# Kernel tuning notes

Hardware: AMD Instinct MI355X
Metric: run time of the kernel (lower is better)

## Reference

```python
import jax, jax.numpy as jnp
import numpy as np

B, S, D, H, DFF = 2, 2048, 768, 12, 3072
DK = D // H
EPS = 1e-6
NEG = -1e9


def setup_inputs() -> dict:
    key = jax.random.key(0)
    ks = jax.random.split(key, 16)
    s = 1.0 / np.sqrt(D)
    inp = {
        'x': jax.random.normal(ks[0], (B, S, D), jnp.float32),
        'wq': jax.random.normal(ks[1], (D, D), jnp.float32) * s,
        'bq': jnp.zeros((D,), jnp.float32),
        'wk': jax.random.normal(ks[2], (D, D), jnp.float32) * s,
        'bk': jnp.zeros((D,), jnp.float32),
        'wv': jax.random.normal(ks[3], (D, D), jnp.float32) * s,
        'bv': jnp.zeros((D,), jnp.float32),
        'wo': jax.random.normal(ks[4], (D, D), jnp.float32) * s,
        'bo': jnp.zeros((D,), jnp.float32),
        'w1': jax.random.normal(ks[5], (D, DFF), jnp.float32) * s,
        'b1': jnp.zeros((DFF,), jnp.float32),
        'w2': jax.random.normal(ks[6], (DFF, D), jnp.float32) * (1.0 / np.sqrt(DFF)),
        'b2': jnp.zeros((D,), jnp.float32),
        'alpha1': jnp.ones((1,), jnp.float32),
        'beta1': jnp.zeros((1,), jnp.float32),
        'alpha2': jnp.ones((1,), jnp.float32),
        'beta2': jnp.zeros((1,), jnp.float32),
        'mask': jax.random.randint(ks[7], (1, 1, S, S), 0, 2, jnp.int32),
    }
    return inp


def layernorm(x, alpha, beta):
    # torch: mean and UNBIASED std (ddof=1), eps added to std (not variance)
    mean = jnp.mean(x, axis=-1, keepdims=True)
    std = jnp.std(x, axis=-1, keepdims=True, ddof=1)
    return alpha * (x - mean) / (std + EPS) + beta


def encoder_layer(x, wq, bq, wk, bk, wv, bv, wo, bo, w1, b1, w2, b2,
                  alpha1, beta1, alpha2, beta2, mask):
    # projections -> [B, H, S, DK]
    def split_heads(t):
        return t.reshape(B, S, H, DK).transpose(0, 2, 1, 3)
    q = split_heads(x @ wq + bq)
    k = split_heads(x @ wk + bk)
    v = split_heads(x @ wv + bv)
    scores = jnp.einsum('bhqd,bhkd->bhqk', q, k) / np.sqrt(DK)  # [B,H,S,S]
    scores = jnp.where(mask == 0, NEG, scores)
    attn = jax.nn.softmax(scores, axis=-1)
    ctx = jnp.einsum('bhqk,bhkd->bhqd', attn, v)
    ctx = ctx.transpose(0, 2, 1, 3).reshape(B, S, D)
    attn_out = ctx @ wo + bo
    x = layernorm(x + attn_out, alpha1, beta1)
    ff = jax.nn.relu(x @ w1 + b1) @ w2 + b2
    x = layernorm(x + ff, alpha2, beta2)
    return x


def reference(x, wq, bq, wk, bk, wv, bv, wo, bo, w1, b1, w2, b2,
              alpha1, beta1, alpha2, beta2, mask):
    return encoder_layer(x, wq, bq, wk, bk, wv, bv, wo, bo, w1, b1, w2, b2,
                         alpha1, beta1, alpha2, beta2, mask)
```

## Files before the change

### kernel.cpp

```cpp
#include <hip/hip_runtime.h>
#include <hip/hip_bf16.h>


typedef short short8 __attribute__((ext_vector_type(8)));
typedef float floatx4 __attribute__((ext_vector_type(4)));
typedef unsigned short ushort_t;
typedef ushort_t ushort4_t __attribute__((ext_vector_type(4)));

#define B_ 2
#define S_ 2048
#define D_ 768
#define H_ 12
#define DK_ 64
#define DFF_ 3072
#define M_ (B_ * S_)
#define RS_ (3 * D_)

#define LOG2E 1.44269504f
#define FMAX_SHIFT 16.0f

__device__ __forceinline__ float bf2f(ushort_t h) {
  union { unsigned int u; float f; } v; v.u = ((unsigned int)h) << 16; return v.f;
}
__device__ __forceinline__ ushort_t f2bf(float f) {
  union { float f; unsigned int u; } v; v.f = f;
  unsigned int u = v.u;
  unsigned int r = (u + 0x7fffu + ((u >> 16) & 1u)) >> 16;
  return (ushort_t)r;
}

__global__ __launch_bounds__(256) void transpose_all_f2b(
    const float* __restrict__ wq, const float* __restrict__ wk,
    const float* __restrict__ wv, const float* __restrict__ wo,
    const float* __restrict__ w1, const float* __restrict__ w2,
    ushort_t* __restrict__ wTqkv, ushort_t* __restrict__ woT,
    ushort_t* __restrict__ w1T, ushort_t* __restrict__ w2T) {
  __shared__ ushort_t t[32][33];
  const int blk = blockIdx.x;
  const float* in; ushort_t* out; int K, N, bx, by;
  if (blk < 2304) {
    const int z = blk / 576, rr = blk % 576;
    in = (z == 0) ? wq : (z == 1) ? wk : (z == 2) ? wv : wo;
    out = (z < 3) ? (wTqkv + (size_t)z * D_ * D_) : woT;
    K = D_; N = D_; bx = rr % 24; by = rr / 24;
  } else if (blk < 4608) {
    const int rr = blk - 2304;
    in = w1; out = w1T; K = D_; N = DFF_; bx = rr % 96; by = rr / 96;
  } else {
    const int rr = blk - 4608;
    in = w2; out = w2T; K = DFF_; N = D_; bx = rr % 24; by = rr / 24;
  }
  const int nt = bx * 32, kt = by * 32;
  const int tx = threadIdx.x & 31, ty = threadIdx.x >> 5;
#pragma unroll
  for (int i = 0; i < 4; i++)
    t[ty + i * 8][tx] = f2bf(in[(size_t)(kt + ty + i * 8) * N + nt + tx]);
  __syncthreads();
#pragma unroll
  for (int i = 0; i < 4; i++)
    out[(size_t)(nt + ty + i * 8) * K + kt + tx] = t[tx][ty + i * 8];
}

__global__ __launch_bounds__(256) void prep_misc(
    const int* __restrict__ mask, ushort_t* __restrict__ maskp,
    const float* __restrict__ x, ushort_t* __restrict__ xb,
    const float* __restrict__ bq, const float* __restrict__ bk,
    const float* __restrict__ bv, float* __restrict__ bqkv) {
  const int blk = blockIdx.x, tid = threadIdx.x;
  if (blk < 2048) {
    const int t = blk * 256 + tid;
    const int q = t >> 8;
    const int cc = t & 255;
    const int k0 = (cc >> 3) * 64;
    const int g = cc & 7, f = g >> 2, lq = g & 3;
    const int* mrow = mask + (size_t)q * S_ + k0;
    const ushort_t cm = f2bf(-1.4427e9f);
    const ushort_t cu = f2bf(-FMAX_SHIFT * LOG2E);
    short8 o;
#pragma unroll
    for (int n2 = 0; n2 < 2; n2++)
#pragma unroll
      for (int r = 0; r < 4; r++) {
        const int kpl = 32 * f + 16 * n2 + 4 * lq + r;
        o[n2 * 4 + r] = (short)((mrow[kpl] == 0) ? cm : cu);
      }
    *(short8*)(maskp + (size_t)q * S_ + k0 + g * 8) = o;
  } else if (blk < 5120) {
    const int i = ((blk - 2048) * 256 + tid) * 4;
#pragma unroll
    for (int j = 0; j < 4; j++) xb[i + j] = f2bf(x[i + j]);
  } else {
    const int i = (blk - 5120) * 256 + tid;
    if (i < 3 * D_)
      bqkv[i] = (i < D_) ? bq[i] : (i < 2 * D_ ? bk[i - D_] : bv[i - 2 * D_]);
  }
}

__global__ __launch_bounds__(256) void vtrans(
    const ushort_t* __restrict__ qkv, ushort_t* __restrict__ vt) {
  __shared__ __align__(16) ushort_t T[64 * 72];
  const int tid = threadIdx.x;
  const int bh = blockIdx.y, b = bh / H_, h = bh % H_;
  const int k0 = blockIdx.x * 64;
  const ushort_t* vbase = qkv + (size_t)(b * S_) * RS_ + 2 * D_ + h * DK_;
#pragma unroll
  for (int i = 0; i < 2; i++) {
    const int idx = tid + i * 256;
    const int r = idx >> 3, c = idx & 7;
    short8 vv = *(const short8*)(vbase + (size_t)(k0 + r) * RS_ + c * 8);
    const int sw = (r >> 3) ^ c;
#pragma unroll
    for (int j = 0; j < 8; j++)
      T[(c * 8 + j) * 72 + sw * 8 + (r & 7)] = (ushort_t)vv[j];
  }
  __syncthreads();
#pragma unroll
  for (int i = 0; i < 2; i++) {
    const int ch = tid + i * 256;
    const int d = ch >> 3, g = ch & 7, f = g >> 2, lq = g & 3;
    short8 o;
#pragma unroll
    for (int n2 = 0; n2 < 2; n2++)
#pragma unroll
      for (int r = 0; r < 4; r++) {
        const int kpl = 32 * f + 16 * n2 + 4 * lq + r;
        o[n2 * 4 + r] = (short)T[d * 72 + (((kpl >> 3) ^ (d >> 3)) * 8) + (kpl & 7)];
      }
    *(short8*)(vt + ((size_t)bh * 64 + d) * S_ + k0 + g * 8) = o;
  }
}

template <int BN, bool SPLIT>
__global__ __launch_bounds__(256) void gemm_bt_t(
    const ushort_t* __restrict__ A, const ushort_t* __restrict__ Bt,
    const float* __restrict__ bias, void* __restrict__ Cv,
    int M, int N, int K, int relu, int qcols, float qscale) {
  constexpr int WN = (BN == 128) ? 2 : 1;
  constexpr int WM = 4 / WN;
  constexpr int FI = 128 / WM / 16;
  constexpr int FJ = BN / WN / 16;
  constexpr int Z = SPLIT ? 2 : 1;
  __shared__ __align__(16) ushort_t Al[2][128 * 32];
  __shared__ __align__(16) ushort_t Bl[2][BN * 32];
  const int tid = threadIdx.x;
  const int w = tid >> 6, lane = tid & 63;
  const int wm = (WN == 2) ? (w >> 1) : w;
  const int wn = (WN == 2) ? (w & 1) : 0;
  const int lq = lane >> 4, lr = lane & 15;

  const int NT_n = N / BN;
  const int mg = M >> 10;
  const int lin = blockIdx.x;
  const int xcd = lin & 7, idx = lin >> 3;
  const int m_t = xcd * mg + idx / (NT_n * Z);
  const int rem = idx % (NT_n * Z);
  const int n_t = rem % NT_n;
  const int z   = rem / NT_n;
  const int m0 = m_t * 128, n0 = n_t * BN;

  int kBeg = 0, kEnd = K;
  if (SPLIT) { const int half = K >> 1; kBeg = z * half; kEnd = kBeg + half; }
  const int NT = (kEnd - kBeg) / 32;

  auto stage = [&](int kt, int s) {
    const int k0 = kBeg + kt * 32;
#pragma unroll
    for (int i = 0; i < 2; i++) {
      const int base = (w * 2 + i) * 512;
      const int e = base + lane * 8;
      const int row = e >> 5, col = e & 31;
      __builtin_amdgcn_global_load_lds(
          (const __attribute__((address_space(1))) void*)(A + (size_t)(m0 + row) * K + k0 + col),
          (__attribute__((address_space(3))) void*)(&Al[s][base]), 16, 0, 0);
    }
#pragma unroll
    for (int i = 0; i < BN / 64; i++) {
      const int base = (w * (BN / 64) + i) * 512;
      const int e = base + lane * 8;
      const int row = e >> 5, col = e & 31;
      __builtin_amdgcn_global_load_lds(
          (const __attribute__((address_space(1))) void*)(Bt + (size_t)(n0 + row) * K + k0 + col),
          (__attribute__((address_space(3))) void*)(&Bl[s][base]), 16, 0, 0);
    }
  };

  floatx4 acc[FI][FJ];
#pragma unroll
  for (int i = 0; i < FI; i++)
#pragma unroll
    for (int j = 0; j < FJ; j++) acc[i][j] = (floatx4){0.f, 0.f, 0.f, 0.f};

  stage(0, 0);
  for (int kt = 0; kt < NT; kt++) {
    const int s = kt & 1;
    __syncthreads();
    if (kt + 1 < NT) stage(kt + 1, s ^ 1);

    short8 af[FI], bf[FJ];
#pragma unroll
    for (int i = 0; i < FI; i++)
      af[i] = *(const short8*)&Al[s][(wm * (FI * 16) + i * 16 + lr) * 32 + lq * 8];
#pragma unroll
    for (int j = 0; j < FJ; j++)
      bf[j] = *(const short8*)&Bl[s][(wn * (FJ * 16) + j * 16 + lr) * 32 + lq * 8];
#pragma unroll
    for (int i = 0; i < FI; i++)
#pragma unroll
      for (int j = 0; j < FJ; j++)
        acc[i][j] = __builtin_amdgcn_mfma_f32_16x16x32_bf16(af[i], bf[j], acc[i][j], 0, 0, 0);
  }

#pragma unroll
  for (int i = 0; i < FI; i++) {
    const int m = m0 + wm * (FI * 16) + i * 16 + lq * 4;
#pragma unroll
    for (int j = 0; j < FJ; j++) {
      const int n = n0 + wn * (FJ * 16) + j * 16 + lr;
      if (SPLIT) {
        ushort_t* P = (ushort_t*)Cv + (size_t)z * M * N;
#pragma unroll
        for (int r = 0; r < 4; r++)
          P[(size_t)(m + r) * N + n] = f2bf(acc[i][j][r]);
      } else {
        const float bv = bias[n];
#pragma unroll
        for (int r = 0; r < 4; r++) {
          float v = acc[i][j][r] + bv;
          if (n < qcols) v *= qscale;
          if (relu) v = v > 0.f ? v : 0.f;
          ((ushort_t*)Cv)[(size_t)(m + r) * N + n] = f2bf(v);
        }
      }
    }
  }
}

__global__ __launch_bounds__(256, 3) void flash_attn(
    const ushort_t* __restrict__ qkv, const ushort_t* __restrict__ vt,
    const ushort_t* __restrict__ maskp, ushort_t* __restrict__ ctx) {
  __shared__ __align__(16) ushort_t lds[2][3][64 * 64];
  const int tid = threadIdx.x;
  const int w = tid >> 6, lane = tid & 63;
  const int wq = w >> 1, wk = w & 1;
  const int lq = lane >> 4, lr = lane & 15;
  const int blk = blockIdx.x;
  const int bh = blk % (B_ * H_), qb = blk / (B_ * H_);
  const int b = bh / H_, h = bh % H_;
  const int q0 = qb * 64;
  const ushort_t* qbase = qkv + (size_t)(b * S_) * RS_ + h * DK_;
  const ushort_t* kbase = qbase + D_;
  const ushort_t* vtb   = vt + (size_t)bh * DK_ * S_;
  const ushort_t* mb    = maskp + (size_t)q0 * S_;

  short8 qfr[2][2];
#pragma unroll
  for (int qf = 0; qf < 2; qf++)
#pragma unroll
    for (int f = 0; f < 2; f++)
      qfr[qf][f] = *(const short8*)(
          qbase + (size_t)(q0 + wq * 32 + qf * 16 + lr) * RS_ + f * 32 + lq * 8);

  auto stage = [&](int k0, int s) {
#pragma unroll
    for (int i = 0; i < 2; i++) {
      const int id = i * 256 + tid;
      const int row = id >> 3;
      const int cc = ((id & 7) ^ (row & 7)) * 8;
      const int dbase = (i * 256 + w * 64) * 8;
      __builtin_amdgcn_global_load_lds(
          (const __attribute__((address_space(1))) void*)(kbase + (size_t)(k0 + row) * RS_ + cc),
          (__attribute__((address_space(3))) void*)(&lds[s][0][dbase]), 16, 0, 0);
      __builtin_amdgcn_global_load_lds(
          (const __attribute__((address_space(1))) void*)(vtb + (size_t)row * S_ + k0 + cc),
          (__attribute__((address_space(3))) void*)(&lds[s][1][dbase]), 16, 0, 0);
      __builtin_amdgcn_global_load_lds(
          (const __attribute__((address_space(1))) void*)(mb + (size_t)row * S_ + k0 + cc),
          (__attribute__((address_space(3))) void*)(&lds[s][2][dbase]), 16, 0, 0);
    }
  };

  floatx4 oacc[2][4], oli[2];
#pragma unroll
  for (int qf = 0; qf < 2; qf++) {
    oli[qf] = (floatx4){0.f, 0.f, 0.f, 0.f};
#pragma unroll
    for (int dt = 0; dt < 4; dt++) oacc[qf][dt] = (floatx4){0.f, 0.f, 0.f, 0.f};
  }
  short8 ones;
#pragma unroll
  for (int j = 0; j < 8; j++) ones[j] = (short)0x3F80;

  stage(0, 0);
  __syncthreads();

  const int sw8 = lr & 7;
  const int c0 = (lq ^ sw8) * 8;
  const int c1 = ((4 + lq) ^ sw8) * 8;
  const int cW = ((4 * wk + lq) ^ sw8) * 8;

  constexpr int NT = S_ / 64;
  for (int t = 0; t < NT; t++) {
    const int s = t & 1;
    if (t + 1 < NT) stage((t + 1) * 64, s ^ 1);

    const ushort_t* kl = &lds[s][0][0];
    const ushort_t* vl = &lds[s][1][0];
    const ushort_t* ml = &lds[s][2][0];

    floatx4 sacc[2][2];
#pragma unroll
    for (int qf = 0; qf < 2; qf++) {
      const short8 bb = *(const short8*)(ml + (wq * 32 + qf * 16 + lr) * 64 + cW);
#pragma unroll
      for (int n2 = 0; n2 < 2; n2++)
#pragma unroll
        for (int r = 0; r < 4; r++)
          sacc[qf][n2][r] = bf2f((ushort_t)bb[n2 * 4 + r]);
    }

#pragma unroll
    for (int n2 = 0; n2 < 2; n2++) {
      const int krow = ((2 * wk + n2) * 16 + lr) * 64;
      short8 a0 = *(const short8*)(kl + krow + c0);
      short8 a1 = *(const short8*)(kl + krow + c1);
#pragma unroll
      for (int qf = 0; qf < 2; qf++) {
        sacc[qf][n2] = __builtin_amdgcn_mfma_f32_16x16x32_bf16(a0, qfr[qf][0], sacc[qf][n2], 0, 0, 0);
        sacc[qf][n2] = __builtin_amdgcn_mfma_f32_16x16x32_bf16(a1, qfr[qf][1], sacc[qf][n2], 0, 0, 0);
      }
    }

    short8 pf[2];
#pragma unroll
    for (int qf = 0; qf < 2; qf++) {
      union { __hip_bfloat162 h2[4]; short8 v; } u;
#pragma unroll
      for (int jj = 0; jj < 4; jj++) {
        const int e0 = jj * 2, e1 = jj * 2 + 1;
        float2 p2;
        p2.x = __builtin_amdgcn_exp2f(sacc[qf][e0 >> 2][e0 & 3]);
        p2.y = __builtin_amdgcn_exp2f(sacc[qf][e1 >> 2][e1 & 3]);
        u.h2[jj] = __float22bfloat162_rn(p2);
      }
      pf[qf] = u.v;
    }

#pragma unroll
    for (int dt = 0; dt < 4; dt++) {
      const short8 vfr = *(const short8*)(vl + (dt * 16 + lr) * 64 + cW);
#pragma unroll
      for (int qf = 0; qf < 2; qf++)
        oacc[qf][dt] = __builtin_amdgcn_mfma_f32_16x16x32_bf16(vfr, pf[qf], oacc[qf][dt], 0, 0, 0);
    }
#pragma unroll
    for (int qf = 0; qf < 2; qf++)
      oli[qf] = __builtin_amdgcn_mfma_f32_16x16x32_bf16(ones, pf[qf], oli[qf], 0, 0, 0);

    __syncthreads();
  }

  float* ex = (float*)&lds[0][0][0];
  if (wk == 1) {
    float* dst = ex + (size_t)(wq * 64 + lane) * 37;
#pragma unroll
    for (int qf = 0; qf < 2; qf++)
#pragma unroll
      for (int dt = 0; dt < 4; dt++)
#pragma unroll
        for (int r = 0; r < 4; r++)
          dst[qf * 16 + dt * 4 + r] = oacc[qf][dt][r];
    dst[32] = oli[0][0];
    dst[33] = oli[1][0];
  }
  __syncthreads();
  if (wk == 0) {
    const float* src = ex + (size_t)(wq * 64 + lane) * 37;
#pragma unroll
    for (int qf = 0; qf < 2; qf++)
#pragma unroll
      for (int dt = 0; dt < 4; dt++)
#pragma unroll
        for (int r = 0; r < 4; r++)
          oacc[qf][dt][r] += src[qf * 16 + dt * 4 + r];
    const float inv0 = 1.f / (oli[0][0] + src[32] + 1e-30f);
    const float inv1 = 1.f / (oli[1][0] + src[33] + 1e-30f);
#pragma unroll
    for (int qf = 0; qf < 2; qf++) {
      const float inv = qf ? inv1 : inv0;
      const size_t row = (size_t)(b * S_ + q0 + wq * 32 + qf * 16 + lr) * D_ + h * DK_;
#pragma unroll
      for (int dt = 0; dt < 4; dt++) {
        ushort4_t o;
#pragma unroll
        for (int r = 0; r < 4; r++) o[r] = f2bf(oacc[qf][dt][r] * inv);
        *(ushort4_t*)(ctx + row + dt * 16 + lq * 4) = o;
      }
    }
  }
}

template <bool XF, bool OF>
__global__ __launch_bounds__(256) void add_ln_comb(
    const void* __restrict__ xv, const ushort_t* __restrict__ P0,
    const ushort_t* __restrict__ P1, const float* __restrict__ cb,
    const float* __restrict__ alpha, const float* __restrict__ beta,
    void* __restrict__ outv) {
  const int row = blockIdx.x, tid = threadIdx.x;
  const int w = tid >> 6, lane = tid & 63;
  __shared__ float red[8];
  float v[3];
#pragma unroll
  for (int i = 0; i < 3; i++) {
    const int c = tid + i * 256;
    const size_t idx = (size_t)row * D_ + c;
    float xv_;
    if (XF) xv_ = ((const float*)xv)[idx];
    else    xv_ = bf2f(((const ushort_t*)xv)[idx]);
    v[i] = xv_ + (bf2f(P0[idx]) + bf2f(P1[idx]) + cb[c]);
  }
  float s = v[0] + v[1] + v[2];
#pragma unroll
  for (int off = 1; off < 64; off <<= 1) s += __shfl_xor(s, off);
  if (lane == 0) red[w] = s;
  __syncthreads();
  const float mean = (red[0] + red[1] + red[2] + red[3]) / (float)D_;
  float d = 0.f;
#pragma unroll
  for (int i = 0; i < 3; i++) { const float t = v[i] - mean; d += t * t; }
#pragma unroll
  for (int off = 1; off < 64; off <<= 1) d += __shfl_xor(d, off);
  if (lane == 0) red[4 + w] = d;
  __syncthreads();
  const float var = (red[4] + red[5] + red[6] + red[7]) / (float)(D_ - 1);
  const float inv = 1.f / (sqrtf(var) + 1e-6f);
  const float a = alpha[0] * inv, bt = beta[0];
#pragma unroll
  for (int i = 0; i < 3; i++) {
    const int c = tid + i * 256;
    const float o = a * (v[i] - mean) + bt;
    if (OF) ((float*)outv)[(size_t)row * D_ + c] = o;
    else    ((ushort_t*)outv)[(size_t)row * D_ + c] = f2bf(o);
  }
}

extern "C" void kernel_launch(void* const* d_in, const int* in_sizes, int n_in,
                              void* d_out, int out_size, void* d_ws, size_t ws_size,
                              hipStream_t stream) {
  const float* x   = (const float*)d_in[0];
  const float* wq  = (const float*)d_in[1];
  const float* bq  = (const float*)d_in[2];
  const float* wk  = (const float*)d_in[3];
  const float* bk  = (const float*)d_in[4];
  const float* wv  = (const float*)d_in[5];
  const float* bv  = (const float*)d_in[6];
  const float* wo  = (const float*)d_in[7];
  const float* bo  = (const float*)d_in[8];
  const float* w1  = (const float*)d_in[9];
  const float* b1  = (const float*)d_in[10];
  const float* w2  = (const float*)d_in[11];
  const float* b2  = (const float*)d_in[12];
  const float* a1  = (const float*)d_in[13];
  const float* be1 = (const float*)d_in[14];
  const float* a2  = (const float*)d_in[15];
  const float* be2 = (const float*)d_in[16];
  const int*   msk = (const int*)d_in[17];

  const size_t E_xb    = 0;
  const size_t E_wTqkv = E_xb    + (size_t)M_ * D_;
  const size_t E_woT   = E_wTqkv + (size_t)3 * D_ * D_;
  const size_t E_w1T   = E_woT   + (size_t)D_ * D_;
  const size_t E_w2T   = E_w1T   + (size_t)DFF_ * D_;
  const size_t E_bqkv  = E_w2T   + (size_t)D_ * DFF_;
  const size_t E_qkv   = E_bqkv  + (size_t)2 * 3 * D_;
  const size_t E_ctx   = E_qkv   + (size_t)M_ * 3 * D_;
  const size_t E_attn  = E_ctx   + (size_t)M_ * D_;
  const size_t E_x1    = E_attn  + (size_t)M_ * D_;
  const size_t E_h1    = E_x1    + (size_t)M_ * D_;
  const size_t E_ff    = E_h1    + (size_t)M_ * DFF_;
  const size_t E_total = E_ff    + (size_t)M_ * D_;
  if (ws_size < E_total * sizeof(ushort_t)) return;

  ushort_t* ws    = (ushort_t*)d_ws;
  ushort_t* xb    = ws + E_xb;
  ushort_t* wTqkv = ws + E_wTqkv;
  ushort_t* woT   = ws + E_woT;
  ushort_t* w1T   = ws + E_w1T;
  ushort_t* w2T   = ws + E_w2T;
  float*    bqkv  = (float*)(ws + E_bqkv);
  ushort_t* qkv   = ws + E_qkv;
  ushort_t* ctx   = ws + E_ctx;
  ushort_t* x1    = ws + E_x1;
  ushort_t* h1    = ws + E_h1;
  ushort_t* maskp = ws + E_h1;
  ushort_t* vt    = ws + E_h1 + (size_t)S_ * S_;
  ushort_t* Pattn = ws + E_h1;
  ushort_t* Pff2  = ws + E_qkv;

  const float SCALE_Q = 0.125f * LOG2E;

  transpose_all_f2b<<<6912, 256, 0, stream>>>(wq, wk, wv, wo, w1, w2,
                                              wTqkv, woT, w1T, w2T);
  prep_misc<<<5129, 256, 0, stream>>>(msk, maskp, x, xb, bq, bk, bv, bqkv);

  gemm_bt_t<64, false><<<1152, 256, 0, stream>>>(
      xb, wTqkv, bqkv, qkv, M_, 3 * D_, D_, 0, D_, SCALE_Q);
  vtrans<<<dim3(S_ / 64, B_ * H_), 256, 0, stream>>>(qkv, vt);
  flash_attn<<<(B_ * H_) * (S_ / 64), 256, 0, stream>>>(qkv, vt, maskp, ctx);
  gemm_bt_t<64, true><<<768, 256, 0, stream>>>(
      ctx, woT, nullptr, Pattn, M_, D_, D_, 0, 0, 1.f);
  add_ln_comb<true, false><<<M_, 256, 0, stream>>>(
      x, Pattn, Pattn + (size_t)M_ * D_, bo, a1, be1, x1);
  gemm_bt_t<64, false><<<1536, 256, 0, stream>>>(
      x1, w1T, b1, h1, M_, DFF_, D_, 1, 0, 1.f);
  gemm_bt_t<64, true><<<768, 256, 0, stream>>>(
      h1, w2T, nullptr, Pff2, M_, D_, DFF_, 0, 0, 1.f);
  add_ln_comb<false, true><<<M_, 256, 0, stream>>>(
      x1, Pff2, Pff2 + (size_t)M_ * D_, b2, a2, be2, d_out);
}
```

Before: 308.2 us.

## Fuse V transpose into QKV GEMM epilogue and retile FFN1 GEMM

The QKV projection GEMM now writes the V columns directly into the transposed, permuted vt layout the attention kernel expects, so the separate vtrans kernel is gone. The FFN1 GEMM switches to a 128-wide N tile with half the blocks. The first residual LayerNorm now reads the bf16 copy of x instead of fp32. The aim is to cut one kernel launch and one V round trip and to improve FFN1 tile reuse. In exchange, the V stores are 8-byte scattered writes and the residual carries bf16 precision.

```diff
diff --git a/kernel.cpp b/kernel.cpp
--- a/kernel.cpp
+++ b/kernel.cpp
@@ -96,44 +96,11 @@
   }
 }
 
-__global__ __launch_bounds__(256) void vtrans(
-    const ushort_t* __restrict__ qkv, ushort_t* __restrict__ vt) {
-  __shared__ __align__(16) ushort_t T[64 * 72];
-  const int tid = threadIdx.x;
-  const int bh = blockIdx.y, b = bh / H_, h = bh % H_;
-  const int k0 = blockIdx.x * 64;
-  const ushort_t* vbase = qkv + (size_t)(b * S_) * RS_ + 2 * D_ + h * DK_;
-#pragma unroll
-  for (int i = 0; i < 2; i++) {
-    const int idx = tid + i * 256;
-    const int r = idx >> 3, c = idx & 7;
-    short8 vv = *(const short8*)(vbase + (size_t)(k0 + r) * RS_ + c * 8);
-    const int sw = (r >> 3) ^ c;
-#pragma unroll
-    for (int j = 0; j < 8; j++)
-      T[(c * 8 + j) * 72 + sw * 8 + (r & 7)] = (ushort_t)vv[j];
-  }
-  __syncthreads();
-#pragma unroll
-  for (int i = 0; i < 2; i++) {
-    const int ch = tid + i * 256;
-    const int d = ch >> 3, g = ch & 7, f = g >> 2, lq = g & 3;
-    short8 o;
-#pragma unroll
-    for (int n2 = 0; n2 < 2; n2++)
-#pragma unroll
-      for (int r = 0; r < 4; r++) {
-        const int kpl = 32 * f + 16 * n2 + 4 * lq + r;
-        o[n2 * 4 + r] = (short)T[d * 72 + (((kpl >> 3) ^ (d >> 3)) * 8) + (kpl & 7)];
-      }
-    *(short8*)(vt + ((size_t)bh * 64 + d) * S_ + k0 + g * 8) = o;
-  }
-}
-
-template <int BN, bool SPLIT>
+template <int BN, bool SPLIT, bool VOUT>
 __global__ __launch_bounds__(256) void gemm_bt_t(
     const ushort_t* __restrict__ A, const ushort_t* __restrict__ Bt,
     const float* __restrict__ bias, void* __restrict__ Cv,
+    ushort_t* __restrict__ vtout,
     int M, int N, int K, int relu, int qcols, float qscale) {
   constexpr int WN = (BN == 128) ? 2 : 1;
   constexpr int WM = 4 / WN;
@@ -221,6 +188,18 @@
 #pragma unroll
         for (int r = 0; r < 4; r++)
           P[(size_t)(m + r) * N + n] = f2bf(acc[i][j][r]);
+      } else if (VOUT && n >= 2 * D_) {
+        const int h = (n - 2 * D_) >> 6, d = (n - 2 * D_) & 63;
+        const int bh = (m >> 11) * H_ + h;
+        const int kp = m & (S_ - 1);
+        const int kw = kp & 63;
+        const int pos = (kp & ~63) + ((kw >> 5) << 5) + (((kw >> 2) & 3) << 3)
+                      + (((kw >> 4) & 1) << 2);
+        const float bv = bias[n];
+        ushort4_t o;
+#pragma unroll
+        for (int r = 0; r < 4; r++) o[r] = f2bf(acc[i][j][r] + bv);
+        *(ushort4_t*)(vtout + ((size_t)bh * DK_ + d) * S_ + pos) = o;
       } else {
         const float bv = bias[n];
 #pragma unroll
@@ -502,18 +481,17 @@
                                               wTqkv, woT, w1T, w2T);
   prep_misc<<<5129, 256, 0, stream>>>(msk, maskp, x, xb, bq, bk, bv, bqkv);
 
-  gemm_bt_t<64, false><<<1152, 256, 0, stream>>>(
-      xb, wTqkv, bqkv, qkv, M_, 3 * D_, D_, 0, D_, SCALE_Q);
-  vtrans<<<dim3(S_ / 64, B_ * H_), 256, 0, stream>>>(qkv, vt);
+  gemm_bt_t<64, false, true><<<1152, 256, 0, stream>>>(
+      xb, wTqkv, bqkv, qkv, vt, M_, 3 * D_, D_, 0, D_, SCALE_Q);
   flash_attn<<<(B_ * H_) * (S_ / 64), 256, 0, stream>>>(qkv, vt, maskp, ctx);
-  gemm_bt_t<64, true><<<768, 256, 0, stream>>>(
-      ctx, woT, nullptr, Pattn, M_, D_, D_, 0, 0, 1.f);
-  add_ln_comb<true, false><<<M_, 256, 0, stream>>>(
-      x, Pattn, Pattn + (size_t)M_ * D_, bo, a1, be1, x1);
-  gemm_bt_t<64, false><<<1536, 256, 0, stream>>>(
-      x1, w1T, b1, h1, M_, DFF_, D_, 1, 0, 1.f);
-  gemm_bt_t<64, true><<<768, 256, 0, stream>>>(
-      h1, w2T, nullptr, Pff2, M_, D_, DFF_, 0, 0, 1.f);
+  gemm_bt_t<64, true, false><<<768, 256, 0, stream>>>(
+      ctx, woT, nullptr, Pattn, nullptr, M_, D_, D_, 0, 0, 1.f);
+  add_ln_comb<false, false><<<M_, 256, 0, stream>>>(
+      xb, Pattn, Pattn + (size_t)M_ * D_, bo, a1, be1, x1);
+  gemm_bt_t<128, false, false><<<768, 256, 0, stream>>>(
+      x1, w1T, b1, h1, nullptr, M_, DFF_, D_, 1, 0, 1.f);
+  gemm_bt_t<64, true, false><<<768, 256, 0, stream>>>(
+      h1, w2T, nullptr, Pff2, nullptr, M_, D_, DFF_, 0, 0, 1.f);
   add_ln_comb<false, true><<<M_, 256, 0, stream>>>(
       x1, Pff2, Pff2 + (size_t)M_ * D_, b2, a2, be2, d_out);
 }
```

New measurement: 293.2 us. -4.9%, faster.
